# Kernel tuning notes

Measured on AMD Instinct MI355X. Metric: run time of the kernel, lower is better.

Reference implementation:

```python
import jax, jax.numpy as jnp
import numpy as np

B, D, N = 8, 1024, 1024
INTER, H = 512, 16
EPS = 1e-5


def conv1x1(x, W, b):
    # x: (B, Cin, N), W: (Cout, Cin), b: (Cout,) -> (B, Cout, N)
    return jnp.einsum('oc,bcn->bon', W, x) + b[None, :, None]


def setup_inputs() -> dict:
    key = jax.random.key(0)
    ks = jax.random.split(key, 12)
    s = 0.02
    v = jax.random.normal(ks[0], (B, D, N), jnp.float32)
    mask = (jax.random.uniform(ks[1], (B, N)) < 0.9).astype(jnp.float32)
    Wg = jax.random.normal(ks[2], (INTER, D), jnp.float32) * s
    bg = jax.random.normal(ks[3], (INTER,), jnp.float32) * s
    Wt = jax.random.normal(ks[4], (INTER, D), jnp.float32) * s
    bt = jax.random.normal(ks[5], (INTER,), jnp.float32) * s
    Wp = jax.random.normal(ks[6], (INTER, D), jnp.float32) * s
    bp = jax.random.normal(ks[7], (INTER,), jnp.float32) * s
    Ww = jax.random.normal(ks[8], (D, INTER), jnp.float32) * s
    bw = jax.random.normal(ks[9], (D,), jnp.float32) * s
    bn_gamma = jax.random.normal(ks[10], (D,), jnp.float32) * s + 1.0
    bn_beta = jax.random.normal(ks[11], (D,), jnp.float32) * s
    bn_mean = jnp.zeros((D,), jnp.float32)
    bn_var = jnp.ones((D,), jnp.float32)
    return {"v": v, "mask": mask, "Wg": Wg, "bg": bg, "Wt": Wt, "bt": bt,
            "Wp": Wp, "bp": bp, "Ww": Ww, "bw": bw, "bn_gamma": bn_gamma,
            "bn_beta": bn_beta, "bn_mean": bn_mean, "bn_var": bn_var}


def reference(v, mask, Wg, bg, Wt, bt, Wp, bp, Ww, bw,
              bn_gamma, bn_beta, bn_mean, bn_var):
    b, d, n = v.shape
    hd = INTER // H  # head dim
    # projections (1x1 conv == per-node linear); move to (B, N, INTER)
    g_v = conv1x1(v, Wg, bg).transpose(0, 2, 1) * mask[:, :, None]
    theta = conv1x1(v, Wt, bt).transpose(0, 2, 1)
    phi = conv1x1(v, Wp, bp).transpose(0, 2, 1)
    theta4 = theta.reshape(b, n, H, hd)  # (B, N, H, hd)
    phi4 = phi.reshape(b, n, H, hd)
    g4 = g_v.reshape(b, n, H, hd)
    # relation matrix R: (B, H, N, N)
    R = jnp.einsum('bnhd,bmhd->bhnm', theta4, phi4)
    C = jnp.sum(mask, axis=1)  # (B,)
    Rm = (R / C[:, None, None, None]) * mask[:, None, :, None] * mask[:, None, None, :]
    # aggregate: (B, N, H, hd)
    y = jnp.einsum('bhnm,bmhd->bnhd', Rm, g4).reshape(b, n, INTER)
    y = y.transpose(0, 2, 1)  # (B, INTER, N)
    # output projection + BatchNorm1d (eval form) + residual
    Wy = conv1x1(y, Ww, bw)
    inv = bn_gamma / jnp.sqrt(bn_var + EPS)
    Wy = (Wy - bn_mean[None, :, None]) * inv[None, :, None] + bn_beta[None, :, None]
    Wy = Wy * mask[:, None, :]
    return Wy + v
```

## Files before the change

kernel.cpp:

```cpp
#include <hip/hip_runtime.h>
#include <hip/hip_bf16.h>
#include <stdint.h>

#define B_ 8
#define D_ 1024
#define N_ 1024
#define INTER_ 512
#define H_ 16
#define EPS_ 1e-5f

typedef __attribute__((ext_vector_type(8))) short bf16x8;
typedef __attribute__((ext_vector_type(4))) float f32x4;
typedef __attribute__((ext_vector_type(4))) unsigned short u16x4;
typedef __attribute__((ext_vector_type(8))) unsigned short u16x8;

__device__ __forceinline__ unsigned short f2bf(float f) {
  union { float f; uint32_t u; } v; v.f = f;
  uint32_t r = (v.u + 0x7FFFu + ((v.u >> 16) & 1u)) >> 16;
  return (unsigned short)r;
}

__device__ __forceinline__ void gload_lds16(const void* g, void* l) {
  __builtin_amdgcn_global_load_lds(
      (const __attribute__((address_space(1))) void*)g,
      (__attribute__((address_space(3))) void*)l, 16, 0, 0);
}

__global__ __launch_bounds__(256) void k_prep(
    const float* __restrict__ v, const float* __restrict__ Wt,
    const float* __restrict__ Wp, const float* __restrict__ Wg,
    const float* __restrict__ Ww, const float* __restrict__ bt,
    const float* __restrict__ bp, const float* __restrict__ bg,
    const float* __restrict__ mask, unsigned short* __restrict__ vT,
    unsigned short* __restrict__ Wall, unsigned short* __restrict__ Wwb,
    float* __restrict__ ball, float* __restrict__ invC) {
  const int blk = blockIdx.x, tid = threadIdx.x;
  if (blk < 2048) {
    __shared__ short T[64 * 72];
    const int b = blk >> 8, tile = blk & 255;
    const int n0 = (tile & 15) * 64, d0 = (tile >> 4) * 64;
    const float* src = v + ((size_t)b * D_ + d0) * N_ + n0;
    const int c = tid & 15, rg = tid >> 4;
#pragma unroll
    for (int i = 0; i < 4; ++i) {
      const int r = rg * 4 + i;
      float4 f = *(const float4*)(src + (size_t)r * N_ + c * 4);
      const int nl = c * 4;
      T[(nl + 0) * 72 + r] = f2bf(f.x);
      T[(nl + 1) * 72 + r] = f2bf(f.y);
      T[(nl + 2) * 72 + r] = f2bf(f.z);
      T[(nl + 3) * 72 + r] = f2bf(f.w);
    }
    __syncthreads();
    unsigned short* dst = vT + ((size_t)b * N_ + n0) * D_ + d0;
    const int ch = tid & 7, nr = tid >> 3;
#pragma unroll
    for (int jj = 0; jj < 2; ++jj) {
      const int nl = nr + jj * 32;
      u16x8 val = *(const u16x8*)&T[nl * 72 + ch * 8];
      *(u16x8*)(dst + (size_t)nl * D_ + ch * 8) = val;
    }
  } else if (blk < 4096) {
    const int idx4 = (blk - 2048) * 256 + tid;
    const int total1 = 1536 * 1024 / 4;
    if (idx4 < total1) {
      const int idx = idx4 * 4;
      const int row = idx >> 10, c = idx & 1023;
      const float* src = row < 512    ? Wt + row * 1024 + c
                         : row < 1024 ? Wp + (row - 512) * 1024 + c
                                      : Wg + (row - 1024) * 1024 + c;
      float4 f = *(const float4*)src;
      u16x4 o = {f2bf(f.x), f2bf(f.y), f2bf(f.z), f2bf(f.w)};
      *(u16x4*)(Wall + idx) = o;
    } else {
      const int idx = (idx4 - total1) * 4;
      float4 f = *(const float4*)(Ww + idx);
      u16x4 o = {f2bf(f.x), f2bf(f.y), f2bf(f.z), f2bf(f.w)};
      *(u16x4*)(Wwb + idx) = o;
    }
  } else if (blk == 4096) {
    for (int i = tid; i < 512; i += 256) {
      ball[i] = bt[i]; ball[512 + i] = bp[i]; ball[1024 + i] = bg[i];
    }
  } else {
    const int b = blk - 4097;
    float s = 0.f;
    for (int i = tid; i < 1024; i += 256) s += mask[b * 1024 + i];
    for (int off = 32; off; off >>= 1) s += __shfl_down(s, off, 64);
    __shared__ float red[4];
    if ((tid & 63) == 0) red[tid >> 6] = s;
    __syncthreads();
    if (tid == 0) invC[b] = 1.0f / (red[0] + red[1] + red[2] + red[3]);
  }
}

#define BM 128
#define BN 128
#define BK 64

__global__ __launch_bounds__(256, 2) void k_gemm1(
    const unsigned short* __restrict__ Wall, const unsigned short* __restrict__ vT,
    const float* __restrict__ ball, const float* __restrict__ mask,
    unsigned short* __restrict__ thT, unsigned short* __restrict__ phi,
    unsigned short* __restrict__ g) {
  __shared__ __align__(16) short smem[128 * 132];
  char* lA = (char*)smem;
  char* lB = lA + 16384;
  const int b = blockIdx.z, bx = blockIdx.x, by = blockIdx.y;
  const int tid = threadIdx.x, lane = tid & 63, w = tid >> 6;
  const int wr = w >> 1, wc = w & 1;

  const unsigned short* Abase = Wall + (size_t)(by * BM) * 1024;
  const unsigned short* Bbase = vT + ((size_t)b * N_ + bx * BN) * 1024;

  const int srow = w * 32 + (lane >> 3);
  const int sgl = lane & 7;

  f32x4 acc[4][4] = {};

  for (int kt = 0; kt < 1024 / BK; ++kt) {
#pragma unroll
    for (int i = 0; i < 4; ++i) {
      const int r = srow + i * 8;
      const int gs = sgl ^ (r & 7);
      gload_lds16(Abase + (size_t)r * 1024 + kt * BK + gs * 8,
                  lA + w * 4096 + i * 1024);
      gload_lds16(Bbase + (size_t)r * 1024 + kt * BK + gs * 8,
                  lB + w * 4096 + i * 1024);
    }
    __syncthreads();
#pragma unroll
    for (int kk = 0; kk < 2; ++kk) {
      bf16x8 af[4], bfr[4];
#pragma unroll
      for (int mf = 0; mf < 4; ++mf) {
        const int r = wr * 64 + mf * 16 + (lane & 15);
        int byte = r * 128 + kk * 64 + ((lane >> 4) * 16);
        byte ^= (r & 7) << 4;
        af[mf] = *(const bf16x8*)(lA + byte);
      }
#pragma unroll
      for (int nf = 0; nf < 4; ++nf) {
        const int r = wc * 64 + nf * 16 + (lane & 15);
        int byte = r * 128 + kk * 64 + ((lane >> 4) * 16);
        byte ^= (r & 7) << 4;
        bfr[nf] = *(const bf16x8*)(lB + byte);
      }
#pragma unroll
      for (int mf = 0; mf < 4; ++mf)
#pragma unroll
        for (int nf = 0; nf < 4; ++nf)
          acc[mf][nf] = __builtin_amdgcn_mfma_f32_16x16x32_bf16(
              af[mf], bfr[nf], acc[mf][nf], 0, 0, 0);
    }
    __syncthreads();
  }

  const int region = by >> 2;
  short* Tc = smem;
  if (region == 0) {
#pragma unroll
    for (int mf = 0; mf < 4; ++mf)
#pragma unroll
      for (int nf = 0; nf < 4; ++nf) {
        const int nl = wc * 64 + nf * 16 + (lane & 15);
        const int ol0 = wr * 64 + mf * 16 + ((lane >> 4) << 2);
        u16x4 o;
#pragma unroll
        for (int r = 0; r < 4; ++r)
          o[r] = f2bf(acc[mf][nf][r] + ball[by * BM + ol0 + r]);
        *(u16x4*)&Tc[nl * 132 + ol0] = o;
      }
  } else {
#pragma unroll
    for (int mf = 0; mf < 4; ++mf)
#pragma unroll
      for (int nf = 0; nf < 4; ++nf) {
        const int nl = wc * 64 + nf * 16 + (lane & 15);
        const int ol0 = wr * 64 + mf * 16 + ((lane >> 4) << 2);
        const float mv = (region == 2) ? mask[b * 1024 + bx * BN + nl] : 1.0f;
#pragma unroll
        for (int r = 0; r < 4; ++r)
          Tc[(ol0 + r) * 132 + nl] =
              f2bf((acc[mf][nf][r] + ball[by * BM + ol0 + r]) * mv);
      }
  }
  __syncthreads();
  const int ch = tid & 15;
#pragma unroll
  for (int j = 0; j < 8; ++j) {
    const int row = (tid >> 4) + j * 16;
    u16x4 lo = *(const u16x4*)&Tc[row * 132 + ch * 8];
    u16x4 hi = *(const u16x4*)&Tc[row * 132 + ch * 8 + 4];
    u16x8 val = {lo[0], lo[1], lo[2], lo[3], hi[0], hi[1], hi[2], hi[3]};
    unsigned short* dst;
    if (region == 0)
      dst = thT + ((size_t)b * N_ + bx * BN + row) * 512 + by * BM + ch * 8;
    else if (region == 1)
      dst = phi + ((size_t)b * 512 + (by - 4) * BM + row) * 1024 + bx * BN + ch * 8;
    else
      dst = g + ((size_t)b * 512 + (by - 8) * BM + row) * 1024 + bx * BN + ch * 8;
    *(u16x8*)dst = val;
  }
}

__global__ __launch_bounds__(256) void k_Spart(const unsigned short* __restrict__ phi,
                                               const unsigned short* __restrict__ g,
                                               float* __restrict__ Spart) {
  const int s = blockIdx.x, h = blockIdx.y, b = blockIdx.z;
  const int tid = threadIdx.x, lane = tid & 63, w = tid >> 6;
  const unsigned short* pb = phi + ((size_t)b * 512 + h * 32) * 1024 + s * 128;
  const unsigned short* gb = g + ((size_t)b * 512 + h * 32) * 1024 + s * 128;
  const int n = w * 32 + ((lane >> 4) * 8);
  bf16x8 af[2], bfr[2];
#pragma unroll
  for (int mf = 0; mf < 2; ++mf)
    af[mf] = *(const bf16x8*)(pb + (size_t)(mf * 16 + (lane & 15)) * 1024 + n);
#pragma unroll
  for (int nf = 0; nf < 2; ++nf)
    bfr[nf] = *(const bf16x8*)(gb + (size_t)(nf * 16 + (lane & 15)) * 1024 + n);
  f32x4 acc[2][2] = {};
#pragma unroll
  for (int mf = 0; mf < 2; ++mf)
#pragma unroll
    for (int nf = 0; nf < 2; ++nf)
      acc[mf][nf] = __builtin_amdgcn_mfma_f32_16x16x32_bf16(
          af[mf], bfr[nf], acc[mf][nf], 0, 0, 0);
  __shared__ float red[4][32][32];
#pragma unroll
  for (int mf = 0; mf < 2; ++mf)
#pragma unroll
    for (int nf = 0; nf < 2; ++nf)
#pragma unroll
      for (int r = 0; r < 4; ++r)
        red[w][mf * 16 + (lane >> 4) * 4 + r][nf * 16 + (lane & 15)] = acc[mf][nf][r];
  __syncthreads();
  float* dst = Spart + ((size_t)(b * 16 + h) * 8 + s) * 1024;
  const int e0 = tid * 4;
  float4 s0 = *(const float4*)(&red[0][0][0] + e0);
  float4 s1 = *(const float4*)(&red[1][0][0] + e0);
  float4 s2 = *(const float4*)(&red[2][0][0] + e0);
  float4 s3 = *(const float4*)(&red[3][0][0] + e0);
  float4 o = {s0.x + s1.x + s2.x + s3.x, s0.y + s1.y + s2.y + s3.y,
              s0.z + s1.z + s2.z + s3.z, s0.w + s1.w + s2.w + s3.w};
  *(float4*)(dst + e0) = o;
}

__global__ __launch_bounds__(256) void k_M(const unsigned short* __restrict__ Wwb,
                                           const float* __restrict__ Spart,
                                           unsigned short* __restrict__ M) {
  const int rb = blockIdx.x, h = blockIdx.y, b = blockIdx.z;
  const int tid = threadIdx.x, lane = tid & 63, w = tid >> 6;
  __shared__ short Sb[32 * 40];
  {
    const int e0 = tid * 4;
    const float* sp = Spart + (size_t)(b * 16 + h) * 8 * 1024 + e0;
    float4 a = {0, 0, 0, 0};
#pragma unroll
    for (int s = 0; s < 8; ++s) {
      float4 p = *(const float4*)(sp + s * 1024);
      a.x += p.x; a.y += p.y; a.z += p.z; a.w += p.w;
    }
    const int row = e0 >> 5, col = e0 & 31;
    u16x4 sv = {f2bf(a.x), f2bf(a.y), f2bf(a.z), f2bf(a.w)};
    *(u16x4*)&Sb[row * 40 + col] = sv;
  }
  __syncthreads();
  const int row0w = rb * 128 + w * 32;
  f32x4 acc[2][2] = {};
  bf16x8 af[2], bfr[2];
#pragma unroll
  for (int mf = 0; mf < 2; ++mf)
    af[mf] = *(const bf16x8*)(Wwb + (size_t)(row0w + mf * 16 + (lane & 15)) * 512 +
                              h * 32 + (lane >> 4) * 8);
#pragma unroll
  for (int nf = 0; nf < 2; ++nf)
    bfr[nf] = *(const bf16x8*)&Sb[(nf * 16 + (lane & 15)) * 40 + (lane >> 4) * 8];
#pragma unroll
  for (int mf = 0; mf < 2; ++mf)
#pragma unroll
    for (int nf = 0; nf < 2; ++nf)
      acc[mf][nf] = __builtin_amdgcn_mfma_f32_16x16x32_bf16(
          af[mf], bfr[nf], acc[mf][nf], 0, 0, 0);
#pragma unroll
  for (int mf = 0; mf < 2; ++mf)
#pragma unroll
    for (int nf = 0; nf < 2; ++nf)
#pragma unroll
      for (int r = 0; r < 4; ++r) {
        const int row = row0w + mf * 16 + (lane >> 4) * 4 + r;
        const int dp = nf * 16 + (lane & 15);
        M[((size_t)b * 1024 + row) * 512 + h * 32 + dp] = f2bf(acc[mf][nf][r]);
      }
}

__global__ __launch_bounds__(256, 2) void k_gemm2(
    const unsigned short* __restrict__ M, const unsigned short* __restrict__ thT,
    const float* __restrict__ mask, const float* __restrict__ invC,
    const float* __restrict__ bw, const float* __restrict__ gamma,
    const float* __restrict__ beta, const float* __restrict__ mean,
    const float* __restrict__ var, const float* __restrict__ vin,
    float* __restrict__ out) {
  __shared__ __align__(16) unsigned short lA[BM * BK];
  __shared__ __align__(16) unsigned short lB[BN * BK];
  const int b = blockIdx.z, bx = blockIdx.x, by = blockIdx.y;
  const int tid = threadIdx.x, lane = tid & 63, w = tid >> 6;
  const int wr = w >> 1, wc = w & 1;

  const unsigned short* Abase = M + ((size_t)b * 1024 + by * BM) * 512;
  const unsigned short* Bbase = thT + ((size_t)b * N_ + bx * BN) * 512;

  const int srow = w * 32 + (lane >> 3);
  const int sgl = lane & 7;

  f32x4 acc[4][4] = {};

  for (int kt = 0; kt < 512 / BK; ++kt) {
#pragma unroll
    for (int i = 0; i < 4; ++i) {
      const int r = srow + i * 8;
      const int gs = sgl ^ (r & 7);
      gload_lds16(Abase + (size_t)r * 512 + kt * BK + gs * 8,
                  (char*)lA + w * 4096 + i * 1024);
      gload_lds16(Bbase + (size_t)r * 512 + kt * BK + gs * 8,
                  (char*)lB + w * 4096 + i * 1024);
    }
    __syncthreads();
#pragma unroll
    for (int kk = 0; kk < 2; ++kk) {
      bf16x8 af[4], bfr[4];
#pragma unroll
      for (int mf = 0; mf < 4; ++mf) {
        const int r = wr * 64 + mf * 16 + (lane & 15);
        int byte = r * 128 + kk * 64 + ((lane >> 4) * 16);
        byte ^= (r & 7) << 4;
        af[mf] = *(const bf16x8*)((const char*)lA + byte);
      }
#pragma unroll
      for (int nf = 0; nf < 4; ++nf) {
        const int r = wc * 64 + nf * 16 + (lane & 15);
        int byte = r * 128 + kk * 64 + ((lane >> 4) * 16);
        byte ^= (r & 7) << 4;
        bfr[nf] = *(const bf16x8*)((const char*)lB + byte);
      }
#pragma unroll
      for (int mf = 0; mf < 4; ++mf)
#pragma unroll
        for (int nf = 0; nf < 4; ++nf)
          acc[mf][nf] = __builtin_amdgcn_mfma_f32_16x16x32_bf16(
              af[mf], bfr[nf], acc[mf][nf], 0, 0, 0);
    }
    __syncthreads();
  }

  const float icb = invC[b];
#pragma unroll
  for (int mf = 0; mf < 4; ++mf) {
#pragma unroll
    for (int nf = 0; nf < 4; ++nf) {
      const int col = bx * BN + wc * 64 + nf * 16 + (lane & 15);
      const int row0 = by * BM + wr * 64 + mf * 16 + ((lane >> 4) << 2);
      const float mv = mask[b * 1024 + col];
      const float sc = mv * icb;
#pragma unroll
      for (int r = 0; r < 4; ++r) {
        const int o = row0 + r;
        float val = acc[mf][nf][r] * sc + bw[o];
        const float inv = gamma[o] * rsqrtf(var[o] + EPS_);
        val = (val - mean[o]) * inv + beta[o];
        const size_t idx = ((size_t)b * 1024 + o) * 1024 + col;
        out[idx] = val * mv + vin[idx];
      }
    }
  }
}

extern "C" void kernel_launch(void* const* d_in, const int* in_sizes, int n_in,
                              void* d_out, int out_size, void* d_ws, size_t ws_size,
                              hipStream_t stream) {
  const float* v = (const float*)d_in[0];
  const float* mask = (const float*)d_in[1];
  const float* Wg = (const float*)d_in[2];
  const float* bg = (const float*)d_in[3];
  const float* Wt = (const float*)d_in[4];
  const float* bt = (const float*)d_in[5];
  const float* Wp = (const float*)d_in[6];
  const float* bp = (const float*)d_in[7];
  const float* Ww = (const float*)d_in[8];
  const float* bw = (const float*)d_in[9];
  const float* gamma = (const float*)d_in[10];
  const float* beta = (const float*)d_in[11];
  const float* mean = (const float*)d_in[12];
  const float* var = (const float*)d_in[13];
  float* out = (float*)d_out;

  char* ws = (char*)d_ws;
  unsigned short* vT = (unsigned short*)ws;    ws += 16777216;
  unsigned short* Wall = (unsigned short*)ws;  ws += 3145728;
  unsigned short* Wwb = (unsigned short*)ws;   ws += 1048576;
  unsigned short* thT = (unsigned short*)ws;   ws += 8388608;
  unsigned short* phi = (unsigned short*)ws;   ws += 8388608;
  unsigned short* g = (unsigned short*)ws;     ws += 8388608;
  float* Spart = (float*)ws;                   ws += 4194304;
  unsigned short* Mw = (unsigned short*)ws;    ws += 8388608;
  float* ball = (float*)ws;                    ws += 6144;
  float* invC = (float*)ws;                    ws += 32;

  k_prep<<<4105, 256, 0, stream>>>(v, Wt, Wp, Wg, Ww, bt, bp, bg, mask,
                                   vT, Wall, Wwb, ball, invC);
  k_gemm1<<<dim3(8, 12, 8), 256, 0, stream>>>(Wall, vT, ball, mask, thT, phi, g);
  k_Spart<<<dim3(8, 16, 8), 256, 0, stream>>>(phi, g, Spart);
  k_M<<<dim3(8, 16, 8), 256, 0, stream>>>(Wwb, Spart, Mw);
  k_gemm2<<<dim3(8, 8, 8), 256, 0, stream>>>(Mw, thT, mask, invC, bw, gamma, beta,
                                             mean, var, v, out);
}
```

Baseline: 176.5 us.

## Fuse phi/g projection with per-head phi·g^T partial reduction in GEMM epilogue

The first projection GEMM now regroups its row tiles so each phi/g block holds 64 phi rows and the matching 64 g rows, covering two heads. Its epilogue computes the per-head phi·g^T partial sums directly from LDS and writes Spart. This removes the separate k_Spart launch and the bf16 phi and g buffers written to and read back from global memory. In exchange, the GEMM epilogue gets longer, with extra syncs and LDS traffic.

```diff
diff --git a/kernel.cpp b/kernel.cpp
--- a/kernel.cpp
+++ b/kernel.cpp
@@ -98,19 +98,25 @@
 #define BN 128
 #define BK 64
 
-__global__ __launch_bounds__(256, 2) void k_gemm1(
+__global__ __launch_bounds__(256, 2) void k_gemmA(
     const unsigned short* __restrict__ Wall, const unsigned short* __restrict__ vT,
     const float* __restrict__ ball, const float* __restrict__ mask,
-    unsigned short* __restrict__ thT, unsigned short* __restrict__ phi,
-    unsigned short* __restrict__ g) {
+    unsigned short* __restrict__ thT, float* __restrict__ Spart) {
   __shared__ __align__(16) short smem[128 * 132];
   char* lA = (char*)smem;
   char* lB = lA + 16384;
   const int b = blockIdx.z, bx = blockIdx.x, by = blockIdx.y;
   const int tid = threadIdx.x, lane = tid & 63, w = tid >> 6;
   const int wr = w >> 1, wc = w & 1;
-
-  const unsigned short* Abase = Wall + (size_t)(by * BM) * 1024;
+  const bool is_theta = (by < 4);
+  const int rg = by - 4;
+
+  const unsigned short* Abase;
+  if (is_theta)
+    Abase = Wall + (size_t)(by * BM) * 1024;
+  else
+    Abase = (w < 2) ? Wall + (size_t)(512 + rg * 64) * 1024
+                    : Wall + (size_t)(1024 + rg * 64 - 64) * 1024;
   const unsigned short* Bbase = vT + ((size_t)b * N_ + bx * BN) * 1024;
 
   const int srow = w * 32 + (lane >> 3);
@@ -156,9 +162,8 @@
     __syncthreads();
   }
 
-  const int region = by >> 2;
   short* Tc = smem;
-  if (region == 0) {
+  if (is_theta) {
 #pragma unroll
     for (int mf = 0; mf < 4; ++mf)
 #pragma unroll
@@ -171,79 +176,76 @@
           o[r] = f2bf(acc[mf][nf][r] + ball[by * BM + ol0 + r]);
         *(u16x4*)&Tc[nl * 132 + ol0] = o;
       }
-  } else {
-#pragma unroll
-    for (int mf = 0; mf < 4; ++mf)
-#pragma unroll
-      for (int nf = 0; nf < 4; ++nf) {
-        const int nl = wc * 64 + nf * 16 + (lane & 15);
-        const int ol0 = wr * 64 + mf * 16 + ((lane >> 4) << 2);
-        const float mv = (region == 2) ? mask[b * 1024 + bx * BN + nl] : 1.0f;
+    __syncthreads();
+    const int ch = tid & 15;
+#pragma unroll
+    for (int j = 0; j < 8; ++j) {
+      const int row = (tid >> 4) + j * 16;
+      u16x4 lo = *(const u16x4*)&Tc[row * 132 + ch * 8];
+      u16x4 hi = *(const u16x4*)&Tc[row * 132 + ch * 8 + 4];
+      u16x8 val = {lo[0], lo[1], lo[2], lo[3], hi[0], hi[1], hi[2], hi[3]};
+      *(u16x8*)(thT + ((size_t)b * N_ + bx * BN + row) * 512 + by * BM + ch * 8) =
+          val;
+    }
+    return;
+  }
+
+#pragma unroll
+  for (int mf = 0; mf < 4; ++mf)
+#pragma unroll
+    for (int nf = 0; nf < 4; ++nf) {
+      const int nl = wc * 64 + nf * 16 + (lane & 15);
+      const int ol0 = wr * 64 + mf * 16 + ((lane >> 4) << 2);
+      const float mv = (wr == 1) ? mask[b * 1024 + bx * BN + nl] : 1.0f;
+      const int gb = (wr == 0) ? 512 + rg * 64 : 1024 + rg * 64 - 64;
+#pragma unroll
+      for (int r = 0; r < 4; ++r)
+        Tc[(ol0 + r) * 132 + nl] =
+            f2bf((acc[mf][nf][r] + ball[gb + ol0 + r]) * mv);
+    }
+  __syncthreads();
+
+  f32x4 accs[2][2][2] = {};
+#pragma unroll
+  for (int hl = 0; hl < 2; ++hl) {
+    bf16x8 af[2], bfr[2];
+#pragma unroll
+    for (int mf = 0; mf < 2; ++mf) {
+      const int row = hl * 32 + mf * 16 + (lane & 15);
+      af[mf] = *(const bf16x8*)&Tc[row * 132 + w * 32 + (lane >> 4) * 8];
+    }
+#pragma unroll
+    for (int nf = 0; nf < 2; ++nf) {
+      const int row = 64 + hl * 32 + nf * 16 + (lane & 15);
+      bfr[nf] = *(const bf16x8*)&Tc[row * 132 + w * 32 + (lane >> 4) * 8];
+    }
+#pragma unroll
+    for (int mf = 0; mf < 2; ++mf)
+#pragma unroll
+      for (int nf = 0; nf < 2; ++nf)
+        accs[hl][mf][nf] = __builtin_amdgcn_mfma_f32_16x16x32_bf16(
+            af[mf], bfr[nf], accs[hl][mf][nf], 0, 0, 0);
+  }
+  __syncthreads();
+  float* red = (float*)smem;
+#pragma unroll
+  for (int hl = 0; hl < 2; ++hl)
+#pragma unroll
+    for (int mf = 0; mf < 2; ++mf)
+#pragma unroll
+      for (int nf = 0; nf < 2; ++nf)
 #pragma unroll
         for (int r = 0; r < 4; ++r)
-          Tc[(ol0 + r) * 132 + nl] =
-              f2bf((acc[mf][nf][r] + ball[by * BM + ol0 + r]) * mv);
-      }
-  }
+          red[((hl * 4 + w) * 32 + mf * 16 + (lane >> 4) * 4 + r) * 32 +
+              nf * 16 + (lane & 15)] = accs[hl][mf][nf][r];
   __syncthreads();
-  const int ch = tid & 15;
-#pragma unroll
-  for (int j = 0; j < 8; ++j) {
-    const int row = (tid >> 4) + j * 16;
-    u16x4 lo = *(const u16x4*)&Tc[row * 132 + ch * 8];
-    u16x4 hi = *(const u16x4*)&Tc[row * 132 + ch * 8 + 4];
-    u16x8 val = {lo[0], lo[1], lo[2], lo[3], hi[0], hi[1], hi[2], hi[3]};
-    unsigned short* dst;
-    if (region == 0)
-      dst = thT + ((size_t)b * N_ + bx * BN + row) * 512 + by * BM + ch * 8;
-    else if (region == 1)
-      dst = phi + ((size_t)b * 512 + (by - 4) * BM + row) * 1024 + bx * BN + ch * 8;
-    else
-      dst = g + ((size_t)b * 512 + (by - 8) * BM + row) * 1024 + bx * BN + ch * 8;
-    *(u16x8*)dst = val;
-  }
-}
-
-__global__ __launch_bounds__(256) void k_Spart(const unsigned short* __restrict__ phi,
-                                               const unsigned short* __restrict__ g,
-                                               float* __restrict__ Spart) {
-  const int s = blockIdx.x, h = blockIdx.y, b = blockIdx.z;
-  const int tid = threadIdx.x, lane = tid & 63, w = tid >> 6;
-  const unsigned short* pb = phi + ((size_t)b * 512 + h * 32) * 1024 + s * 128;
-  const unsigned short* gb = g + ((size_t)b * 512 + h * 32) * 1024 + s * 128;
-  const int n = w * 32 + ((lane >> 4) * 8);
-  bf16x8 af[2], bfr[2];
-#pragma unroll
-  for (int mf = 0; mf < 2; ++mf)
-    af[mf] = *(const bf16x8*)(pb + (size_t)(mf * 16 + (lane & 15)) * 1024 + n);
-#pragma unroll
-  for (int nf = 0; nf < 2; ++nf)
-    bfr[nf] = *(const bf16x8*)(gb + (size_t)(nf * 16 + (lane & 15)) * 1024 + n);
-  f32x4 acc[2][2] = {};
-#pragma unroll
-  for (int mf = 0; mf < 2; ++mf)
-#pragma unroll
-    for (int nf = 0; nf < 2; ++nf)
-      acc[mf][nf] = __builtin_amdgcn_mfma_f32_16x16x32_bf16(
-          af[mf], bfr[nf], acc[mf][nf], 0, 0, 0);
-  __shared__ float red[4][32][32];
-#pragma unroll
-  for (int mf = 0; mf < 2; ++mf)
-#pragma unroll
-    for (int nf = 0; nf < 2; ++nf)
-#pragma unroll
-      for (int r = 0; r < 4; ++r)
-        red[w][mf * 16 + (lane >> 4) * 4 + r][nf * 16 + (lane & 15)] = acc[mf][nf][r];
-  __syncthreads();
-  float* dst = Spart + ((size_t)(b * 16 + h) * 8 + s) * 1024;
-  const int e0 = tid * 4;
-  float4 s0 = *(const float4*)(&red[0][0][0] + e0);
-  float4 s1 = *(const float4*)(&red[1][0][0] + e0);
-  float4 s2 = *(const float4*)(&red[2][0][0] + e0);
-  float4 s3 = *(const float4*)(&red[3][0][0] + e0);
-  float4 o = {s0.x + s1.x + s2.x + s3.x, s0.y + s1.y + s2.y + s3.y,
-              s0.z + s1.z + s2.z + s3.z, s0.w + s1.w + s2.w + s3.w};
-  *(float4*)(dst + e0) = o;
+  for (int e = tid; e < 2048; e += 256) {
+    const int hl = e >> 10, idx = e & 1023;
+    const float* rb = red + (hl * 4) * 1024;
+    const float sum = rb[idx] + rb[1024 + idx] + rb[2048 + idx] + rb[3072 + idx];
+    const int h = rg * 2 + hl;
+    Spart[(((size_t)b * 16 + h) * 8 + bx) * 1024 + idx] = sum;
+  }
 }
 
 __global__ __launch_bounds__(256) void k_M(const unsigned short* __restrict__ Wwb,
@@ -399,8 +401,6 @@
   unsigned short* Wall = (unsigned short*)ws;  ws += 3145728;
   unsigned short* Wwb = (unsigned short*)ws;   ws += 1048576;
   unsigned short* thT = (unsigned short*)ws;   ws += 8388608;
-  unsigned short* phi = (unsigned short*)ws;   ws += 8388608;
-  unsigned short* g = (unsigned short*)ws;     ws += 8388608;
   float* Spart = (float*)ws;                   ws += 4194304;
   unsigned short* Mw = (unsigned short*)ws;    ws += 8388608;
   float* ball = (float*)ws;                    ws += 6144;
@@ -408,8 +408,7 @@
 
   k_prep<<<4105, 256, 0, stream>>>(v, Wt, Wp, Wg, Ww, bt, bp, bg, mask,
                                    vT, Wall, Wwb, ball, invC);
-  k_gemm1<<<dim3(8, 12, 8), 256, 0, stream>>>(Wall, vT, ball, mask, thT, phi, g);
-  k_Spart<<<dim3(8, 16, 8), 256, 0, stream>>>(phi, g, Spart);
+  k_gemmA<<<dim3(8, 12, 8), 256, 0, stream>>>(Wall, vT, ball, mask, thT, Spart);
   k_M<<<dim3(8, 16, 8), 256, 0, stream>>>(Wwb, Spart, Mw);
   k_gemm2<<<dim3(8, 8, 8), 256, 0, stream>>>(Mw, thT, mask, invC, bw, gamma, beta,
                                              mean, var, v, out);
```

Result: faster. 171.0 us (-3.1%).
